# Kernel optimization log

Measured on AMD Instinct MI355X. Metric: run time of the kernel, lower is better.

The kernel has to match this reference:

```python
import jax, jax.numpy as jnp
import numpy as np

B, T, C, L = 64, 1000, 128, 100  # batch, frames, classes (blank=C-1), max label len
NEG = jnp.float32(-1e30)


def setup_inputs() -> dict:
    key = jax.random.key(0)
    k0, k1, k2, k3 = jax.random.split(key, 4)
    # ctc_batch_cost expects softmax probabilities
    y_pred = jax.nn.softmax(jax.random.normal(k0, (B, T, C), dtype=jnp.float32), axis=-1)
    y_true = jax.random.randint(k1, (B, L), 0, C - 1).astype(jnp.int32)  # labels exclude blank
    label_lengths = jax.random.randint(k2, (B,), L // 2, L + 1).astype(jnp.int32)
    input_lengths = jax.random.randint(k3, (B,), T // 2, T + 1).astype(jnp.int32)
    return {"y_true": y_true, "y_pred": y_pred,
            "input_lengths": input_lengths, "label_lengths": label_lengths}


def _ctc_loss(y_true, y_pred, input_lengths, label_lengths):
    # Keras: logits = log(y_pred + epsilon), blank index = C-1
    logp = jnp.log(y_pred + 1e-7)                     # [B,T,C]
    blank = C - 1
    S = 2 * L + 1
    # extended label sequence: blank, l1, blank, l2, ..., blank  -> [B,S]
    ext = jnp.full((B, S), blank, dtype=jnp.int32).at[:, 1::2].set(y_true)
    # gather per-extended-position log probs: [B,T,S]
    logp_ext = jnp.take_along_axis(logp, jnp.broadcast_to(ext[:, None, :], (B, T, S)), axis=2)
    # skip (s-2) transition allowed when ext[s] != blank and ext[s] != ext[s-2]
    ext_m2 = jnp.concatenate([jnp.full((B, 2), blank, jnp.int32), ext[:, :-2]], axis=1)
    skip = (ext != blank) & (ext != ext_m2)           # [B,S]

    alpha0 = jnp.full((B, S), NEG, dtype=logp.dtype)
    alpha0 = alpha0.at[:, 0].set(logp_ext[:, 0, 0]).at[:, 1].set(logp_ext[:, 0, 1])

    def step(alpha, xs):
        lp_t, t = xs                                   # lp_t [B,S]
        a1 = jnp.concatenate([jnp.full((B, 1), NEG, alpha.dtype), alpha[:, :-1]], axis=1)
        a2 = jnp.concatenate([jnp.full((B, 2), NEG, alpha.dtype), alpha[:, :-2]], axis=1)
        a2 = jnp.where(skip, a2, NEG)
        new = jnp.logaddexp(jnp.logaddexp(alpha, a1), a2) + lp_t
        # freeze alpha past each sample's input length
        alpha = jnp.where(t < input_lengths[:, None], new, alpha)
        return alpha, None

    xs = (jnp.moveaxis(logp_ext, 1, 0)[1:], jnp.arange(1, T))
    alpha, _ = jax.lax.scan(step, alpha0, xs)
    # final positions: S_b-1 = 2*label_len, S_b-2 = 2*label_len - 1
    a_last = jnp.take_along_axis(alpha, (2 * label_lengths)[:, None], axis=1)[:, 0]
    a_prev = jnp.take_along_axis(alpha, (2 * label_lengths - 1)[:, None], axis=1)[:, 0]
    return -jnp.logaddexp(a_last, a_prev)[:, None]     # [B,1] like ctc_batch_cost


def reference(y_true, y_pred, input_lengths, label_lengths):
    return _ctc_loss(y_true, y_pred, input_lengths, label_lengths)
```

## Files before the change

### kernel.cpp

```cpp
#include <hip/hip_runtime.h>

#define B_ 64
#define T_ 1000
#define C_ 128
#define L_ 100
#define BLANK 127
#define LN2F 0.69314718055994530942f
#define PH 64
#define NPROD 8
#define FSTRIDE 1024
#define BUFSZ (PH * FSTRIDE)

__device__ __forceinline__ float flog2(float x) { return __builtin_amdgcn_logf(x); }
__device__ __forceinline__ float frcp(float x)  { return __builtin_amdgcn_rcpf(x); }

#define DPP_ROW_SHR1   0x111
#define DPP_ROW_SHR2   0x112
#define DPP_ROW_SHR4   0x114
#define DPP_ROW_SHR8   0x118
#define DPP_WAVE_SHR1  0x138
#define DPP_WAVE_SHL1  0x130

template <int CTRL>
__device__ __forceinline__ int dpp_mov(int src) {
    return __builtin_amdgcn_update_dpp(0, src, CTRL, 0xF, 0xF, false);
}

__global__ __launch_bounds__(576) void ctc_split_kernel(
    const int* __restrict__ y_true, const float* __restrict__ y_pred,
    const int* __restrict__ in_len, const int* __restrict__ lab_len,
    double* __restrict__ AVf, double* __restrict__ AVb,
    double* __restrict__ Ls, int* __restrict__ Es)
{
    const int bb    = blockIdx.x & 63;
    const bool isB  = blockIdx.x >= 64;
    const int tid   = threadIdx.x;
    const int l     = tid & 63;
    const int wv    = tid >> 6;

    __shared__ __align__(16) char ldsb[2 * BUFSZ];
    __shared__ float lgs[2][NPROD];

    const int k1 = min(2 * l, L_ - 1);
    const int k3 = min(2 * l + 1, L_ - 1);
    const int e1 = y_true[bb * L_ + k1];
    const int e3 = y_true[bb * L_ + k3];
    const double m1 = (k1 == 0 || e1 != y_true[bb * L_ + k1 - 1]) ? 1.0 : 0.0;
    const double m3 = (e3 != y_true[bb * L_ + k3 - 1]) ? 1.0 : 0.0;
    const int k1n = min(2 * l + 2, L_ - 1);
    const double m1n = (y_true[bb * L_ + k1n] != y_true[bb * L_ + k1n - 1]) ? 1.0 : 0.0;

    const int Teff = min(T_, in_len[bb]);
    const int N    = Teff - 1;
    const int Hf   = (N + 1) >> 1;
    const int Hb   = N - Hf;
    const int steps_total = isB ? Hb : Hf;
    const int P_full = steps_total >> 6;
    const int rem    = steps_total & 63;
    const int P      = P_full + (rem ? 1 : 0);
    const float* rowb = y_pred + (size_t)bb * T_ * C_;

    double a0 = 0.0, a1 = 0.0, a2 = 0.0, a3 = 0.0;
    double Lsum = 0.0;
    int E = 0;

    const int fs = (wv - 1) * 8;

    auto fillw = [&](int phf) {
        char* bbw = ldsb + (phf & 1) * BUFSZ;
        const int kb_ = phf * PH + fs;
        float g10,g30,gb0, g11,g31,gb1, g12,g32,gb2, g13,g33,gb3,
              g14,g34,gb4, g15,g35,gb5, g16,g36,gb6, g17,g37,gb7;
        int t0_,t1_,t2_,t3_,t4_,t5_,t6_,t7_;
#define FR(i_) (isB ? (N - (kb_ + i_)) : (1 + kb_ + i_))
        t0_=FR(0); t1_=FR(1); t2_=FR(2); t3_=FR(3);
        t4_=FR(4); t5_=FR(5); t6_=FR(6); t7_=FR(7);
#undef FR
        {
            const float* r_;
            r_ = rowb + (size_t)min(max(t0_,1),N) * C_; g10=r_[e1]; g30=r_[e3]; gb0=r_[BLANK];
            r_ = rowb + (size_t)min(max(t1_,1),N) * C_; g11=r_[e1]; g31=r_[e3]; gb1=r_[BLANK];
            r_ = rowb + (size_t)min(max(t2_,1),N) * C_; g12=r_[e1]; g32=r_[e3]; gb2=r_[BLANK];
            r_ = rowb + (size_t)min(max(t3_,1),N) * C_; g13=r_[e1]; g33=r_[e3]; gb3=r_[BLANK];
            r_ = rowb + (size_t)min(max(t4_,1),N) * C_; g14=r_[e1]; g34=r_[e3]; gb4=r_[BLANK];
            r_ = rowb + (size_t)min(max(t5_,1),N) * C_; g15=r_[e1]; g35=r_[e3]; gb5=r_[BLANK];
            r_ = rowb + (size_t)min(max(t6_,1),N) * C_; g16=r_[e1]; g36=r_[e3]; gb6=r_[BLANK];
            r_ = rowb + (size_t)min(max(t7_,1),N) * C_; g17=r_[e1]; g37=r_[e3]; gb7=r_[BLANK];
        }
        __builtin_amdgcn_sched_barrier(0);
        float lgs_ = 0.f;
#define PWR(i_, T_V, G1, G3, GB) { \
        float rb_ = GB + 1e-7f; \
        float rc_ = frcp(rb_); \
        char* q_ = bbw + (fs + i_) * FSTRIDE; \
        *(double2*)(q_ + 16 * l) = make_double2((double)((G1 + 1e-7f) * rc_), \
                                                 (double)((G3 + 1e-7f) * rc_)); \
        bool ok_ = isB ? (T_V >= Hf + 1 && T_V <= N) : (T_V >= 1 && T_V <= Hf); \
        lgs_ += ok_ ? flog2(rb_) : 0.f; }
        PWR(0, t0_, g10, g30, gb0); PWR(1, t1_, g11, g31, gb1);
        PWR(2, t2_, g12, g32, gb2); PWR(3, t3_, g13, g33, gb3);
        PWR(4, t4_, g14, g34, gb4); PWR(5, t5_, g15, g35, gb5);
        PWR(6, t6_, g16, g36, gb6); PWR(7, t7_, g17, g37, gb7);
#undef PWR
        if (l == 0) lgs[phf & 1][wv - 1] = lgs_;
    };

#define DECLF(Pr) double Pr##q1, Pr##q3
#define DECLB(Pr) double Pr##q1, Pr##q3, Pr##q1n
#define LDF(Pr, fi_) { \
    double2 v_ = *(const double2*)(bbp_ + (fi_) * FSTRIDE + 16 * l); \
    Pr##q1 = v_.x; Pr##q3 = v_.y; }
#define LDFB(Pr, fi_) { \
    double2 v_ = *(const double2*)(bbp_ + (fi_) * FSTRIDE + 16 * l); \
    Pr##q1 = v_.x; Pr##q3 = v_.y; \
    Pr##q1n = *(const double*)(bbp_ + (fi_) * FSTRIDE + 16 * ((l + 1) & 63)); }

#define STEPQ(Pr) { \
    int slo_ = dpp_mov<DPP_WAVE_SHR1>(__double2loint(a3)); \
    int shi_ = dpp_mov<DPP_WAVE_SHR1>(__double2hiint(a3)); \
    double pm1_ = __hiloint2double(shi_, slo_); \
    double n0_ = a0 + pm1_; \
    double n1_ = (a1 + a0 + m1 * pm1_) * Pr##q1; \
    double n2_ = a2 + a1; \
    double n3_ = (a3 + a2 + m3 * a1) * Pr##q3; \
    a0 = n0_; a1 = n1_; a2 = n2_; a3 = n3_; }

#define STEPB(Pr) { \
    int n0lo_ = dpp_mov<DPP_WAVE_SHL1>(__double2loint(a0)); \
    int n0hi_ = dpp_mov<DPP_WAVE_SHL1>(__double2hiint(a0)); \
    int n1lo_ = dpp_mov<DPP_WAVE_SHL1>(__double2loint(a1)); \
    int n1hi_ = dpp_mov<DPP_WAVE_SHL1>(__double2hiint(a1)); \
    double b0n_ = __hiloint2double(n0hi_, n0lo_); \
    double b1n_ = __hiloint2double(n1hi_, n1lo_); \
    double c1_ = a1 * Pr##q1; \
    double c3_ = a3 * Pr##q3; \
    double c1n_ = b1n_ * Pr##q1n; \
    double n0_ = a0 + c1_; \
    double n1_ = c1_ + a2 + m3 * c3_; \
    double n2_ = a2 + c3_; \
    double n3_ = c3_ + b0n_ + m1n * c1n_; \
    a0 = n0_; a1 = n1_; a2 = n2_; a3 = n3_; }

#define DPPMAX(u_, ctrl_) { unsigned t_ = (unsigned)dpp_mov<ctrl_>((int)(u_)); \
    u_ = max(u_, t_); }
#define RESCALE() { \
    unsigned u_ = max(max((unsigned)__double2hiint(a0), (unsigned)__double2hiint(a1)), \
                      max((unsigned)__double2hiint(a2), (unsigned)__double2hiint(a3))); \
    DPPMAX(u_, DPP_ROW_SHR1); \
    DPPMAX(u_, DPP_ROW_SHR2); \
    DPPMAX(u_, DPP_ROW_SHR4); \
    DPPMAX(u_, DPP_ROW_SHR8); \
    unsigned g_ = max(max((unsigned)__builtin_amdgcn_readlane((int)u_, 15), \
                          (unsigned)__builtin_amdgcn_readlane((int)u_, 31)), \
                      max((unsigned)__builtin_amdgcn_readlane((int)u_, 47), \
                          (unsigned)__builtin_amdgcn_readlane((int)u_, 63))); \
    int kk_ = (int)(g_ >> 20); \
    if (kk_ > 0) { \
        double f_ = __hiloint2double((2046 - kk_) << 20, 0); \
        a0 *= f_; a1 *= f_; a2 *= f_; a3 *= f_; \
        E += kk_ - 1023; } }

#define BODY32F(base_) { \
    const char* bbp_ = (base_); \
    DECLF(A0); DECLF(A1); DECLF(A2); DECLF(A3); \
    DECLF(B0); DECLF(B1); DECLF(B2); DECLF(B3); \
    LDF(A0,0); LDF(A1,1); LDF(A2,2); LDF(A3,3); \
    LDF(B0,4); LDF(B1,5); LDF(B2,6); LDF(B3,7); \
    STEPQ(A0); STEPQ(A1); STEPQ(A2); STEPQ(A3); \
    LDF(A0,8); LDF(A1,9); LDF(A2,10); LDF(A3,11); \
    STEPQ(B0); STEPQ(B1); STEPQ(B2); STEPQ(B3); \
    LDF(B0,12); LDF(B1,13); LDF(B2,14); LDF(B3,15); \
    STEPQ(A0); STEPQ(A1); STEPQ(A2); STEPQ(A3); \
    LDF(A0,16); LDF(A1,17); LDF(A2,18); LDF(A3,19); \
    STEPQ(B0); STEPQ(B1); STEPQ(B2); STEPQ(B3); RESCALE(); \
    LDF(B0,20); LDF(B1,21); LDF(B2,22); LDF(B3,23); \
    STEPQ(A0); STEPQ(A1); STEPQ(A2); STEPQ(A3); \
    LDF(A0,24); LDF(A1,25); LDF(A2,26); LDF(A3,27); \
    STEPQ(B0); STEPQ(B1); STEPQ(B2); STEPQ(B3); \
    LDF(B0,28); LDF(B1,29); LDF(B2,30); LDF(B3,31); \
    STEPQ(A0); STEPQ(A1); STEPQ(A2); STEPQ(A3); \
    STEPQ(B0); STEPQ(B1); STEPQ(B2); STEPQ(B3); RESCALE(); }

#define BODY32B(base_) { \
    const char* bbp_ = (base_); \
    DECLB(A0); DECLB(A1); DECLB(A2); DECLB(A3); \
    DECLB(B0); DECLB(B1); DECLB(B2); DECLB(B3); \
    LDFB(A0,0); LDFB(A1,1); LDFB(A2,2); LDFB(A3,3); \
    LDFB(B0,4); LDFB(B1,5); LDFB(B2,6); LDFB(B3,7); \
    STEPB(A0); STEPB(A1); STEPB(A2); STEPB(A3); \
    LDFB(A0,8); LDFB(A1,9); LDFB(A2,10); LDFB(A3,11); \
    STEPB(B0); STEPB(B1); STEPB(B2); STEPB(B3); \
    LDFB(B0,12); LDFB(B1,13); LDFB(B2,14); LDFB(B3,15); \
    STEPB(A0); STEPB(A1); STEPB(A2); STEPB(A3); \
    LDFB(A0,16); LDFB(A1,17); LDFB(A2,18); LDFB(A3,19); \
    STEPB(B0); STEPB(B1); STEPB(B2); STEPB(B3); RESCALE(); \
    LDFB(B0,20); LDFB(B1,21); LDFB(B2,22); LDFB(B3,23); \
    STEPB(A0); STEPB(A1); STEPB(A2); STEPB(A3); \
    LDFB(A0,24); LDFB(A1,25); LDFB(A2,26); LDFB(A3,27); \
    STEPB(B0); STEPB(B1); STEPB(B2); STEPB(B3); \
    LDFB(B0,28); LDFB(B1,29); LDFB(B2,30); LDFB(B3,31); \
    STEPB(A0); STEPB(A1); STEPB(A2); STEPB(A3); \
    STEPB(B0); STEPB(B1); STEPB(B2); STEPB(B3); RESCALE(); }

    if (wv >= 1) {
        fillw(0);
    } else if (!isB) {
        __builtin_amdgcn_s_setprio(1);
        float pb0_ = rowb[BLANK] + 1e-7f;
        float p10_ = rowb[e1]    + 1e-7f;
        a0 = (l == 0) ? 1.0 : 0.0;
        a1 = (l == 0) ? (double)(p10_ / pb0_) : 0.0;
        Lsum = (double)flog2(pb0_);
    } else {
        __builtin_amdgcn_s_setprio(1);
        const int llb = lab_len[bb];
        const int pa = 2 * llb, pq = 2 * llb - 1;
        a0 = (4 * l     == pa) ? 1.0 : 0.0;
        a1 = (4 * l + 1 == pq) ? 1.0 : 0.0;
        a2 = (4 * l + 2 == pa) ? 1.0 : 0.0;
        a3 = (4 * l + 3 == pq) ? 1.0 : 0.0;
    }
    __syncthreads();

    for (int ph = 0; ph < P; ++ph) {
        if (wv >= 1) {
            if (ph + 1 < P) fillw(ph + 1);
        } else {
            const char* base_ = ldsb + (ph & 1) * BUFSZ;
            const int steps = (ph < P_full) ? 64 : rem;
            if (steps == 64) {
                if (!isB) { BODY32F(base_); BODY32F(base_ + 32 * FSTRIDE); }
                else      { BODY32B(base_); BODY32B(base_ + 32 * FSTRIDE); }
            } else {
                const char* bbp_ = base_;
                if (!isB) {
                    for (int k_ = 0; k_ < steps; ++k_) {
                        DECLF(Tq); LDF(Tq, k_); STEPQ(Tq);
                        if ((k_ & 15) == 15) RESCALE();
                    }
                } else {
                    for (int k_ = 0; k_ < steps; ++k_) {
                        DECLB(Tq); LDFB(Tq, k_); STEPB(Tq);
                        if ((k_ & 15) == 15) RESCALE();
                    }
                }
                RESCALE();
            }
            float lg_ = 0.f;
            #pragma unroll
            for (int w_ = 0; w_ < NPROD; ++w_) lg_ += lgs[ph & 1][w_];
            Lsum += (double)lg_;
        }
        __syncthreads();
    }

    if (wv == 0) {
        double* AV = (isB ? AVb : AVf) + bb * 256;
        AV[4 * l + 0] = a0; AV[4 * l + 1] = a1;
        AV[4 * l + 2] = a2; AV[4 * l + 3] = a3;
        if (l == 0) {
            Ls[bb * 2 + (isB ? 1 : 0)] = Lsum;
            Es[bb * 2 + (isB ? 1 : 0)] = E;
        }
    }
}

__global__ __launch_bounds__(64) void ctc_combine_kernel(
    const double* __restrict__ AVf, const double* __restrict__ AVb,
    const double* __restrict__ Ls, const int* __restrict__ Es,
    float* __restrict__ out)
{
    const int b = blockIdx.x;
    const int l = threadIdx.x;
    const double* f = AVf + b * 256;
    const double* g = AVb + b * 256;
    double d = f[4*l+0]*g[4*l+0] + f[4*l+1]*g[4*l+1]
             + f[4*l+2]*g[4*l+2] + f[4*l+3]*g[4*l+3];
    d += __shfl_xor(d, 1);  d += __shfl_xor(d, 2);  d += __shfl_xor(d, 4);
    d += __shfl_xor(d, 8);  d += __shfl_xor(d, 16); d += __shfl_xor(d, 32);
    if (l == 0) {
        double Ltot = Ls[b * 2] + Ls[b * 2 + 1];
        int    Etot = Es[b * 2] + Es[b * 2 + 1];
        int hi = __double2hiint(d), lo = __double2loint(d);
        int ke = (hi >> 20) & 0x7FF;
        double mant = __hiloint2double((hi & 0x000FFFFF) | (1023 << 20), lo);
        float r = flog2((float)mant) + (float)(ke - 1023 + Etot) + (float)Ltot;
        out[b] = -r * LN2F;
    }
}

extern "C" void kernel_launch(void* const* d_in, const int* in_sizes, int n_in,
                              void* d_out, int out_size, void* d_ws, size_t ws_size,
                              hipStream_t stream) {
    const int*   y_true  = (const int*)d_in[0];
    const float* y_pred  = (const float*)d_in[1];
    const int*   in_len  = (const int*)d_in[2];
    const int*   lab_len = (const int*)d_in[3];
    float*       out     = (float*)d_out;

    double* AVf = (double*)d_ws;
    double* AVb = AVf + 64 * 256;
    double* Ls  = AVb + 64 * 256;
    int*    Es  = (int*)(Ls + 128);

    ctc_split_kernel<<<128, 576, 0, stream>>>(y_true, y_pred, in_len, lab_len,
                                              AVf, AVb, Ls, Es);
    ctc_combine_kernel<<<64, 64, 0, stream>>>(AVf, AVb, Ls, Es, out);
}
```

Baseline: 33.74 us.

## Fuse combine kernel into split kernel via last-block atomic counter

Removes the separate combine kernel launch. The last block to finish, found with an atomic counter reset by a memset, computes all 64 batch losses. The change also halves rescale frequency in the full-phase bodies to every 32 steps and unrolls the remainder loop by 4. The risks are a memset launch that replaces the kernel launch, a serialized tail in a single block, and a larger exponent range between rescales.

Measured after the change: 52.57 us. 55.8% more time.

```diff
diff --git a/kernel.cpp b/kernel.cpp
--- a/kernel.cpp
+++ b/kernel.cpp
@@ -30,7 +30,8 @@
     const int* __restrict__ y_true, const float* __restrict__ y_pred,
     const int* __restrict__ in_len, const int* __restrict__ lab_len,
     double* __restrict__ AVf, double* __restrict__ AVb,
-    double* __restrict__ Ls, int* __restrict__ Es)
+    double* __restrict__ Ls, int* __restrict__ Es,
+    int* __restrict__ ctr, float* __restrict__ out)
 {
     const int bb    = blockIdx.x & 63;
     const bool isB  = blockIdx.x >= 64;
@@ -40,6 +41,7 @@
 
     __shared__ __align__(16) char ldsb[2 * BUFSZ];
     __shared__ float lgs[2][NPROD];
+    __shared__ int lastFlag;
 
     const int k1 = min(2 * l, L_ - 1);
     const int k3 = min(2 * l + 1, L_ - 1);
@@ -172,7 +174,7 @@
     LDF(B0,12); LDF(B1,13); LDF(B2,14); LDF(B3,15); \
     STEPQ(A0); STEPQ(A1); STEPQ(A2); STEPQ(A3); \
     LDF(A0,16); LDF(A1,17); LDF(A2,18); LDF(A3,19); \
-    STEPQ(B0); STEPQ(B1); STEPQ(B2); STEPQ(B3); RESCALE(); \
+    STEPQ(B0); STEPQ(B1); STEPQ(B2); STEPQ(B3); \
     LDF(B0,20); LDF(B1,21); LDF(B2,22); LDF(B3,23); \
     STEPQ(A0); STEPQ(A1); STEPQ(A2); STEPQ(A3); \
     LDF(A0,24); LDF(A1,25); LDF(A2,26); LDF(A3,27); \
@@ -193,7 +195,7 @@
     LDFB(B0,12); LDFB(B1,13); LDFB(B2,14); LDFB(B3,15); \
     STEPB(A0); STEPB(A1); STEPB(A2); STEPB(A3); \
     LDFB(A0,16); LDFB(A1,17); LDFB(A2,18); LDFB(A3,19); \
-    STEPB(B0); STEPB(B1); STEPB(B2); STEPB(B3); RESCALE(); \
+    STEPB(B0); STEPB(B1); STEPB(B2); STEPB(B3); \
     LDFB(B0,20); LDFB(B1,21); LDFB(B2,22); LDFB(B3,23); \
     STEPB(A0); STEPB(A1); STEPB(A2); STEPB(A3); \
     LDFB(A0,24); LDFB(A1,25); LDFB(A2,26); LDFB(A3,27); \
@@ -233,15 +235,26 @@
                 else      { BODY32B(base_); BODY32B(base_ + 32 * FSTRIDE); }
             } else {
                 const char* bbp_ = base_;
+                int k_ = 0;
                 if (!isB) {
-                    for (int k_ = 0; k_ < steps; ++k_) {
+                    for (; k_ + 4 <= steps; k_ += 4) {
+                        DECLF(T0); DECLF(T1); DECLF(T2); DECLF(T3);
+                        LDF(T0, k_); LDF(T1, k_ + 1); LDF(T2, k_ + 2); LDF(T3, k_ + 3);
+                        STEPQ(T0); STEPQ(T1); STEPQ(T2); STEPQ(T3);
+                        if ((k_ & 31) == 28) RESCALE();
+                    }
+                    for (; k_ < steps; ++k_) {
                         DECLF(Tq); LDF(Tq, k_); STEPQ(Tq);
-                        if ((k_ & 15) == 15) RESCALE();
                     }
                 } else {
-                    for (int k_ = 0; k_ < steps; ++k_) {
+                    for (; k_ + 4 <= steps; k_ += 4) {
+                        DECLB(T0); DECLB(T1); DECLB(T2); DECLB(T3);
+                        LDFB(T0, k_); LDFB(T1, k_ + 1); LDFB(T2, k_ + 2); LDFB(T3, k_ + 3);
+                        STEPB(T0); STEPB(T1); STEPB(T2); STEPB(T3);
+                        if ((k_ & 31) == 28) RESCALE();
+                    }
+                    for (; k_ < steps; ++k_) {
                         DECLB(Tq); LDFB(Tq, k_); STEPB(Tq);
-                        if ((k_ & 15) == 15) RESCALE();
                     }
                 }
                 RESCALE();
@@ -263,29 +276,38 @@
             Es[bb * 2 + (isB ? 1 : 0)] = E;
         }
     }
-}
-
-__global__ __launch_bounds__(64) void ctc_combine_kernel(
-    const double* __restrict__ AVf, const double* __restrict__ AVb,
-    const double* __restrict__ Ls, const int* __restrict__ Es,
-    float* __restrict__ out)
-{
-    const int b = blockIdx.x;
-    const int l = threadIdx.x;
-    const double* f = AVf + b * 256;
-    const double* g = AVb + b * 256;
-    double d = f[4*l+0]*g[4*l+0] + f[4*l+1]*g[4*l+1]
-             + f[4*l+2]*g[4*l+2] + f[4*l+3]*g[4*l+3];
-    d += __shfl_xor(d, 1);  d += __shfl_xor(d, 2);  d += __shfl_xor(d, 4);
-    d += __shfl_xor(d, 8);  d += __shfl_xor(d, 16); d += __shfl_xor(d, 32);
-    if (l == 0) {
-        double Ltot = Ls[b * 2] + Ls[b * 2 + 1];
-        int    Etot = Es[b * 2] + Es[b * 2 + 1];
-        int hi = __double2hiint(d), lo = __double2loint(d);
-        int ke = (hi >> 20) & 0x7FF;
-        double mant = __hiloint2double((hi & 0x000FFFFF) | (1023 << 20), lo);
-        float r = flog2((float)mant) + (float)(ke - 1023 + Etot) + (float)Ltot;
-        out[b] = -r * LN2F;
+    __threadfence();
+    __syncthreads();
+    if (tid == 0) {
+        int old = atomicAdd(ctr, 1);
+        lastFlag = (old == 127) ? 1 : 0;
+    }
+    __syncthreads();
+
+    if (lastFlag) {
+        __threadfence();
+        const int w = tid >> 6;
+        if (w < 8) {
+            #pragma unroll
+            for (int i_ = 0; i_ < 8; ++i_) {
+                const int bi = w * 8 + i_;
+                const double* f = AVf + bi * 256;
+                const double* g = AVb + bi * 256;
+                double d = f[4*l+0]*g[4*l+0] + f[4*l+1]*g[4*l+1]
+                         + f[4*l+2]*g[4*l+2] + f[4*l+3]*g[4*l+3];
+                d += __shfl_xor(d, 1);  d += __shfl_xor(d, 2);  d += __shfl_xor(d, 4);
+                d += __shfl_xor(d, 8);  d += __shfl_xor(d, 16); d += __shfl_xor(d, 32);
+                if (l == 0) {
+                    double Ltot = Ls[bi * 2] + Ls[bi * 2 + 1];
+                    int    Etot = Es[bi * 2] + Es[bi * 2 + 1];
+                    int hi = __double2hiint(d), lo = __double2loint(d);
+                    int ke = (hi >> 20) & 0x7FF;
+                    double mant = __hiloint2double((hi & 0x000FFFFF) | (1023 << 20), lo);
+                    float r = flog2((float)mant) + (float)(ke - 1023 + Etot) + (float)Ltot;
+                    out[bi] = -r * LN2F;
+                }
+            }
+        }
     }
 }
 
@@ -302,8 +324,9 @@
     double* AVb = AVf + 64 * 256;
     double* Ls  = AVb + 64 * 256;
     int*    Es  = (int*)(Ls + 128);
-
+    int*    ctr = Es + 128;
+
+    hipMemsetAsync(ctr, 0, sizeof(int), stream);
     ctc_split_kernel<<<128, 576, 0, stream>>>(y_true, y_pred, in_len, lab_len,
-                                              AVf, AVb, Ls, Es);
-    ctc_combine_kernel<<<64, 64, 0, stream>>>(AVf, AVb, Ls, Es, out);
+                                              AVf, AVb, Ls, Es, ctr, out);
 }
```
